# Optimization experiments

Hardware: AMD Instinct MI355X
Metric: run time of the kernel (lower is better)

The kernel has to match this reference:

```python
import jax, jax.numpy as jnp
import numpy as np

# config constants
H = 2048          # hidden_size
I_MOE = 1408      # moe_intermediate_size
E = 8             # n_routed_experts
TOP_K = 2         # num_experts_per_tok
NG = 4            # n_group
TOPK_G = 2        # topk_group
SCALE = 2.5       # routed_scaling_factor
N_SHARED = 2      # n_shared_experts
I_SHARED = I_MOE * N_SHARED
B, S = 1, 2048


def setup_inputs() -> dict:
    key = jax.random.key(0)
    ks = jax.random.split(key, 9)
    sc = 0.02
    return {
        "x": jax.random.normal(ks[0], (B, S, H), dtype=jnp.float32),
        "router_weight": jax.random.normal(ks[1], (E, H), dtype=jnp.float32) * sc,
        "e_score_correction_bias": jnp.zeros((E,), dtype=jnp.float32),
        "gate_w": jax.random.normal(ks[2], (E, I_MOE, H), dtype=jnp.float32) * sc,
        "up_w": jax.random.normal(ks[3], (E, I_MOE, H), dtype=jnp.float32) * sc,
        "down_w": jax.random.normal(ks[4], (E, H, I_MOE), dtype=jnp.float32) * sc,
        "shared_gate_w": jax.random.normal(ks[5], (I_SHARED, H), dtype=jnp.float32) * sc,
        "shared_up_w": jax.random.normal(ks[6], (I_SHARED, H), dtype=jnp.float32) * sc,
        "shared_down_w": jax.random.normal(ks[7], (H, I_SHARED), dtype=jnp.float32) * sc,
    }


def _mlp(x, gw, uw, dw):
    # SwiGLU MLP: down( silu(gate(x)) * up(x) )
    return (jax.nn.silu(x @ gw.T) * (x @ uw.T)) @ dw.T


def _route(x2d, rw, bias):
    T = x2d.shape[0]
    logits = x2d.astype(jnp.float32) @ rw.astype(jnp.float32).T          # [T,E]
    scores = jax.nn.sigmoid(logits)                                       # [T,E]
    sfc = scores + bias[None, :]                                          # [T,E]
    # group scores: sum of top-2 per group
    grp = sfc.reshape(T, NG, E // NG)
    group_scores = jnp.sum(jax.lax.top_k(grp, 2)[0], axis=-1)             # [T,NG]
    grp_idx = jax.lax.top_k(group_scores, TOPK_G)[1]                      # [T,topk_group]
    group_mask = jnp.zeros((T, NG), jnp.float32).at[
        jnp.arange(T)[:, None], grp_idx].set(1.0)                         # [T,NG]
    score_mask = jnp.repeat(group_mask, E // NG, axis=1)                  # [T,E]
    masked = jnp.where(score_mask > 0, sfc, 0.0)
    topk_idx = jax.lax.top_k(masked, TOP_K)[1]                            # [T,K]
    topk_w = jnp.take_along_axis(scores, topk_idx, axis=1)                # [T,K]
    topk_w = topk_w / (jnp.sum(topk_w, axis=-1, keepdims=True) + 1e-20)   # norm_topk_prob
    return topk_idx, topk_w * SCALE


def reference(x, router_weight, e_score_correction_bias, gate_w, up_w, down_w,
              shared_gate_w, shared_up_w, shared_down_w):
    orig_shape = x.shape
    x2d = x.reshape(-1, H)                                                # [T,H]
    T = x2d.shape[0]
    topk_idx, topk_w = _route(x2d, router_weight, e_score_correction_bias)
    # per-token per-expert combine weights [T,E] (top-k indices are distinct per token)
    cw = jnp.zeros((T, E), jnp.float32).at[
        jnp.arange(T)[:, None], topk_idx].add(topk_w)

    def expert_body(acc, ws):
        gw, uw, dw, cwe = ws  # gw/uw:[I,H], dw:[H,I], cwe:[T]
        y = _mlp(x2d, gw, uw, dw)
        return acc + cwe[:, None] * y, None

    routed, _ = jax.lax.scan(expert_body, jnp.zeros_like(x2d),
                             (gate_w, up_w, down_w, cw.T))
    out = routed.reshape(orig_shape) + _mlp(x, shared_gate_w, shared_up_w, shared_down_w)
    return out
```

## Files before the change

### kernel.cpp

```cpp
#include <hip/hip_runtime.h>
#include <hip/hip_bf16.h>
#include <math.h>

#define H 2048
#define IMOE 1408
#define NEXP 8
#define T_TOK 2048
#define ISH 2816
#define SCALEF 2.5f

#define NT_GU_R (IMOE / 64)
#define NT_GU_S (ISH / 64)
#define NT_DN   (H / 128)
#define GU_GRID (39 * NT_GU_R + 16 * NT_GU_S)
#define DN_GRID (39 * NT_DN + 16 * NT_DN)

typedef __attribute__((ext_vector_type(8))) short short8;
typedef __attribute__((ext_vector_type(4))) short short4v;
typedef __attribute__((ext_vector_type(4))) float floatx4;

__device__ inline float b2f(short v) {
    unsigned int u = ((unsigned int)(unsigned short)v) << 16;
    float f; __builtin_memcpy(&f, &u, 4); return f;
}
__device__ inline short f2b(float f) {
    __hip_bfloat16 h = __float2bfloat16(f);
    short s; __builtin_memcpy(&s, &h, 2); return s;
}

__device__ __forceinline__ void async16(const short* g, short* l) {
    __builtin_amdgcn_global_load_lds(
        (const __attribute__((address_space(1))) unsigned*)g,
        (__attribute__((address_space(3))) unsigned*)l, 16, 0, 0);
}

__device__ __forceinline__ int xcd_map(int orig, int nwg) {
    int q = nwg >> 3, r = nwg & 7;
    int x = orig & 7, s = orig >> 3;
    int base = (x < r) ? x * (q + 1) : r * (q + 1) + (x - r) * q;
    return base + s;
}

__global__ __launch_bounds__(256) void router_kernel(
    const float* __restrict__ x, const float* __restrict__ rw,
    const float* __restrict__ bias,
    int* __restrict__ cnt, int* __restrict__ tokList, int* __restrict__ slotList,
    float* __restrict__ pairW)
{
    const int wid  = (blockIdx.x * 256 + threadIdx.x) >> 6;
    const int lane = threadIdx.x & 63;
    if (wid >= T_TOK) return;
    const float* xr = x + (size_t)wid * H;

    float acc[NEXP];
#pragma unroll
    for (int e = 0; e < NEXP; ++e) acc[e] = 0.f;

#pragma unroll
    for (int c = 0; c < 8; ++c) {
        int idx = (c * 64 + lane) * 4;
        floatx4 xv = *(const floatx4*)(xr + idx);
#pragma unroll
        for (int e = 0; e < NEXP; ++e) {
            floatx4 wv = *(const floatx4*)(rw + e * H + idx);
            acc[e] += xv.x * wv.x + xv.y * wv.y + xv.z * wv.z + xv.w * wv.w;
        }
    }
#pragma unroll
    for (int e = 0; e < NEXP; ++e)
        for (int off = 32; off; off >>= 1)
            acc[e] += __shfl_xor(acc[e], off, 64);

    if (lane == 0) {
        float s[NEXP], sfc[NEXP];
#pragma unroll
        for (int e = 0; e < NEXP; ++e) {
            s[e]   = 1.0f / (1.0f + expf(-acc[e]));
            sfc[e] = s[e] + bias[e];
        }
        float gs[4];
#pragma unroll
        for (int g = 0; g < 4; ++g) gs[g] = sfc[2 * g] + sfc[2 * g + 1];
        int g1 = 0;
        for (int g = 1; g < 4; ++g) if (gs[g] > gs[g1]) g1 = g;
        int g2 = -1;
        for (int g = 0; g < 4; ++g) {
            if (g == g1) continue;
            if (g2 < 0 || gs[g] > gs[g2]) g2 = g;
        }
        float msk[NEXP];
#pragma unroll
        for (int e = 0; e < NEXP; ++e) {
            int g = e >> 1;
            msk[e] = (g == g1 || g == g2) ? sfc[e] : 0.0f;
        }
        int e1 = 0;
        for (int e = 1; e < NEXP; ++e) if (msk[e] > msk[e1]) e1 = e;
        int e2 = -1;
        for (int e = 0; e < NEXP; ++e) {
            if (e == e1) continue;
            if (e2 < 0 || msk[e] > msk[e2]) e2 = e;
        }
        float w1 = s[e1], w2 = s[e2];
        float inv = SCALEF / (w1 + w2 + 1e-20f);
        w1 *= inv; w2 *= inv;
        int p1 = atomicAdd(&cnt[e1], 1);
        tokList[e1 * T_TOK + p1]  = wid;
        slotList[e1 * T_TOK + p1] = 2 * wid;
        pairW[2 * wid] = w1;
        int p2 = atomicAdd(&cnt[e2], 1);
        tokList[e2 * T_TOK + p2]  = wid;
        slotList[e2 * T_TOK + p2] = 2 * wid + 1;
        pairW[2 * wid + 1] = w2;
    }
}

__global__ void plan_kernel(const int* __restrict__ cnt, int* __restrict__ meta)
{
    if (blockIdx.x != 0 || threadIdx.x != 0) return;
    int base = 0, gu = 0, dn = 0;
    meta[20] = 0; meta[32] = 0;
    for (int e = 0; e < NEXP; ++e) {
        int M = cnt[e];
        meta[e] = M;
        meta[9 + e] = base;
        base += M;
        int MT = (M + 127) >> 7;
        gu += MT * NT_GU_R;
        dn += MT * NT_DN;
        meta[21 + e] = gu;
        meta[33 + e] = dn;
    }
    meta[8]  = T_TOK;
    meta[17] = 0;
    meta[29] = gu + 16 * NT_GU_S;
    meta[41] = dn + 16 * NT_DN;
}

__global__ __launch_bounds__(256) void convert_kernel(
    const float* __restrict__ src, short* __restrict__ dst, int n4)
{
    int idx = blockIdx.x * 256 + threadIdx.x;
    int stride = gridDim.x * 256;
    for (; idx < n4; idx += stride) {
        floatx4 v = *(const floatx4*)(src + (size_t)idx * 4);
        short4v o = { f2b(v.x), f2b(v.y), f2b(v.z), f2b(v.w) };
        *(short4v*)(dst + (size_t)idx * 4) = o;
    }
}

#define W8_GU  2883584
#define W8_SH  720896
#define W8_S1  (W8_GU)
#define W8_S2  (2*W8_GU)
#define W8_S3  (3*W8_GU)
#define W8_S4  (3*W8_GU + W8_SH)
#define W8_S5  (3*W8_GU + 2*W8_SH)
#define W8_S6  (3*W8_GU + 3*W8_SH)
__global__ __launch_bounds__(256) void wconvert_kernel(
    const float* __restrict__ gw, const float* __restrict__ uw,
    const float* __restrict__ dw, const float* __restrict__ sgw,
    const float* __restrict__ suw, const float* __restrict__ sdw,
    short* __restrict__ gwb, short* __restrict__ uwb, short* __restrict__ dwb,
    short* __restrict__ sgwb, short* __restrict__ suwb, short* __restrict__ sdwb)
{
    int idx = blockIdx.x * 256 + threadIdx.x;
    int stride = gridDim.x * 256;
    for (; idx < W8_S6; idx += stride) {
        const float* s; short* d; int local;
        if (idx < W8_S3) {
            if (idx < W8_S1)      { s = gw;  d = gwb;  local = idx; }
            else if (idx < W8_S2) { s = uw;  d = uwb;  local = idx - W8_S1; }
            else                  { s = dw;  d = dwb;  local = idx - W8_S2; }
        } else {
            if (idx < W8_S4)      { s = sgw; d = sgwb; local = idx - W8_S3; }
            else if (idx < W8_S5) { s = suw; d = suwb; local = idx - W8_S4; }
            else                  { s = sdw; d = sdwb; local = idx - W8_S5; }
        }
        floatx4 v0 = *(const floatx4*)(s + (size_t)local * 8);
        floatx4 v1 = *(const floatx4*)(s + (size_t)local * 8 + 4);
        short8 o = { f2b(v0.x), f2b(v0.y), f2b(v0.z), f2b(v0.w),
                     f2b(v1.x), f2b(v1.y), f2b(v1.z), f2b(v1.w) };
        *(short8*)(d + (size_t)local * 8) = o;
    }
}

__global__ __launch_bounds__(256) void gu_gemm(
    const short* __restrict__ xb,
    const short* __restrict__ gwb, const short* __restrict__ uwb,
    const short* __restrict__ sgwb, const short* __restrict__ suwb,
    short* __restrict__ hiddenP, short* __restrict__ hiddenS,
    const int* __restrict__ tokList, const int* __restrict__ meta)
{
    const int total = meta[29];
    if (blockIdx.x >= total) return;
    const int idx = xcd_map(blockIdx.x, total);
    int e = 0;
    while (e < 8 && idx >= meta[21 + e]) ++e;

    int M, NT, Nout, rowBase;
    const short *b1, *b2;
    const int* gat;
    short* outP;
    if (e < 8) {
        M = meta[e]; NT = NT_GU_R; Nout = IMOE; rowBase = meta[9 + e];
        b1 = gwb + (size_t)e * IMOE * H;
        b2 = uwb + (size_t)e * IMOE * H;
        gat = tokList + e * T_TOK;
        outP = hiddenP;
    } else {
        M = T_TOK; NT = NT_GU_S; Nout = ISH; rowBase = 0;
        b1 = sgwb; b2 = suwb; gat = nullptr; outP = hiddenS;
    }
    const int MT = (M + 127) >> 7;
    const int local = idx - meta[20 + e];
    const int mt = local % MT;
    const int nt = local / MT;

    __shared__ short As[128 * 64];
    __shared__ short Bgu[128 * 64];

    const int tid  = threadIdx.x;
    const int w    = tid >> 6;
    const int lane = tid & 63;
    const int quad = lane >> 4;
    const int l16  = lane & 15;
    const int wm = w >> 1, wn = w & 1;

    const int r8 = lane >> 3;
    const int cs = (lane & 7) ^ r8;
    const short* aSrc[4];
    const short* bSrc[4];
    short* ldsA[4];
    short* ldsB[4];
#pragma unroll
    for (int i = 0; i < 4; ++i) {
        int r = w * 32 + i * 8 + r8;
        int p = mt * 128 + r;
        int pos = p < M ? p : (M - 1);
        int arow = gat ? gat[pos] : pos;
        aSrc[i] = xb + (size_t)arow * H + cs * 8;
        ldsA[i] = As + (w * 32 + i * 8) * 64;
        const short* wsrc = (r < 64) ? (b1 + (size_t)(nt * 64 + r) * H)
                                     : (b2 + (size_t)(nt * 64 + r - 64) * H);
        bSrc[i] = wsrc + cs * 8;
        ldsB[i] = Bgu + (w * 32 + i * 8) * 64;
    }

    floatx4 accg[4][2] = {};
    floatx4 accu[4][2] = {};

    for (int k0 = 0; k0 < H; k0 += 64) {
#pragma unroll
        for (int i = 0; i < 4; ++i) async16(aSrc[i] + k0, ldsA[i]);
#pragma unroll
        for (int i = 0; i < 4; ++i) async16(bSrc[i] + k0, ldsB[i]);
        __syncthreads();
        const int sw = l16 & 7;
        short8 af[4], bgf[2], buf[2];
#pragma unroll
        for (int kk2 = 0; kk2 < 2; ++kk2) {
            const int c = kk2 * 4 + quad;
#pragma unroll
            for (int m = 0; m < 4; ++m)
                af[m] = *(const short8*)(As + (wm * 64 + m * 16 + l16) * 64 + (c ^ sw) * 8);
#pragma unroll
            for (int n = 0; n < 2; ++n) {
                bgf[n] = *(const short8*)(Bgu + (wn * 32 + n * 16 + l16) * 64 + (c ^ sw) * 8);
                buf[n] = *(const short8*)(Bgu + (64 + wn * 32 + n * 16 + l16) * 64 + (c ^ sw) * 8);
            }
#pragma unroll
            for (int m = 0; m < 4; ++m)
#pragma unroll
                for (int n = 0; n < 2; ++n) {
                    accg[m][n] = __builtin_amdgcn_mfma_f32_16x16x32_bf16(af[m], bgf[n], accg[m][n], 0, 0, 0);
                    accu[m][n] = __builtin_amdgcn_mfma_f32_16x16x32_bf16(af[m], buf[n], accu[m][n], 0, 0, 0);
                }
        }
        __syncthreads();
    }

#pragma unroll
    for (int m = 0; m < 4; ++m) {
#pragma unroll
        for (int rr = 0; rr < 4; ++rr) {
            int lr = wm * 64 + m * 16 + quad * 4 + rr;
            int p = mt * 128 + lr;
            if (p >= M) continue;
            size_t rowoff = (size_t)(rowBase + p) * Nout + nt * 64 + wn * 32;
#pragma unroll
            for (int n = 0; n < 2; ++n) {
                float g = accg[m][n][rr];
                float u = accu[m][n][rr];
                outP[rowoff + n * 16 + l16] = f2b(g / (1.0f + __expf(-g)) * u);
            }
        }
    }
}

__global__ __launch_bounds__(256) void dn_gemm(
    const short* __restrict__ hiddenP, const short* __restrict__ hiddenS,
    const short* __restrict__ dwb, const short* __restrict__ sdwb,
    short* __restrict__ outPairs, short* __restrict__ sharedOut,
    const int* __restrict__ slotList, const int* __restrict__ meta)
{
    const int total = meta[41];
    if (blockIdx.x >= total) return;
    const int rtot = meta[40];
    int idx;
    if (blockIdx.x < rtot) idx = xcd_map(blockIdx.x, rtot);
    else                   idx = rtot + xcd_map(blockIdx.x - rtot, total - rtot);
    int e = 0;
    while (e < 8 && idx >= meta[33 + e]) ++e;

    int M, K, rowBase;
    const short* bp;
    const short* Abase;
    const int* scat;
    short* outP;
    if (e < 8) {
        M = meta[e]; K = IMOE; rowBase = meta[9 + e];
        bp = dwb + (size_t)e * H * IMOE;
        Abase = hiddenP; scat = slotList + e * T_TOK; outP = outPairs;
    } else {
        M = T_TOK; K = ISH; rowBase = 0;
        bp = sdwb; Abase = hiddenS; scat = nullptr; outP = sharedOut;
    }
    const int MT = (M + 127) >> 7;
    const int local = idx - meta[32 + e];
    const int mt = local % MT;
    const int nt = local / MT;

    __shared__ short As[128 * 64];
    __shared__ short Bs[128 * 64];

    const int tid  = threadIdx.x;
    const int w    = tid >> 6;
    const int lane = tid & 63;
    const int quad = lane >> 4;
    const int l16  = lane & 15;
    const int wm = w >> 1, wn = w & 1;

    const int r8 = lane >> 3;
    const int cs = (lane & 7) ^ r8;
    const short* aSrc[4];
    const short* bSrc[4];
    short* ldsA[4];
    short* ldsB[4];
#pragma unroll
    for (int i = 0; i < 4; ++i) {
        int r = w * 32 + i * 8 + r8;
        int p = mt * 128 + r;
        int pos = p < M ? p : (M - 1);
        aSrc[i] = Abase + (size_t)(rowBase + pos) * K + cs * 8;
        ldsA[i] = As + (w * 32 + i * 8) * 64;
        bSrc[i] = bp + (size_t)(nt * 128 + r) * K + cs * 8;
        ldsB[i] = Bs + (w * 32 + i * 8) * 64;
    }

    floatx4 acc[4][4] = {};

    const int kIters = K >> 6;
    for (int kt = 0; kt < kIters; ++kt) {
        const int k0 = kt << 6;
#pragma unroll
        for (int i = 0; i < 4; ++i) async16(aSrc[i] + k0, ldsA[i]);
#pragma unroll
        for (int i = 0; i < 4; ++i) async16(bSrc[i] + k0, ldsB[i]);
        __syncthreads();
        const int sw = l16 & 7;
        short8 af[4], bf[4];
#pragma unroll
        for (int kk2 = 0; kk2 < 2; ++kk2) {
            const int c = kk2 * 4 + quad;
#pragma unroll
            for (int m = 0; m < 4; ++m)
                af[m] = *(const short8*)(As + (wm * 64 + m * 16 + l16) * 64 + (c ^ sw) * 8);
#pragma unroll
            for (int n = 0; n < 4; ++n)
                bf[n] = *(const short8*)(Bs + (wn * 64 + n * 16 + l16) * 64 + (c ^ sw) * 8);
#pragma unroll
            for (int m = 0; m < 4; ++m)
#pragma unroll
                for (int n = 0; n < 4; ++n)
                    acc[m][n] = __builtin_amdgcn_mfma_f32_16x16x32_bf16(af[m], bf[n], acc[m][n], 0, 0, 0);
        }
        __syncthreads();
    }

#pragma unroll
    for (int m = 0; m < 4; ++m) {
#pragma unroll
        for (int rr = 0; rr < 4; ++rr) {
            int lr = wm * 64 + m * 16 + quad * 4 + rr;
            int p = mt * 128 + lr;
            if (p >= M) continue;
            int crow = scat ? scat[p] : p;
            size_t rowoff = (size_t)crow * H + nt * 128 + wn * 64;
#pragma unroll
            for (int n = 0; n < 4; ++n)
                outP[rowoff + n * 16 + l16] = f2b(acc[m][n][rr]);
        }
    }
}

__global__ __launch_bounds__(256) void combine_kernel(
    const short* __restrict__ outPairs, const short* __restrict__ sharedOut,
    const float* __restrict__ pairW, float* __restrict__ out)
{
    size_t gi = ((size_t)blockIdx.x * 256 + threadIdx.x) * 8;
    int t = (int)(gi >> 11);
    int h = (int)(gi & (H - 1));
    float w0 = pairW[2 * t], w1 = pairW[2 * t + 1];
    short8 p0 = *(const short8*)(outPairs + (size_t)(2 * t) * H + h);
    short8 p1 = *(const short8*)(outPairs + (size_t)(2 * t + 1) * H + h);
    short8 sh = *(const short8*)(sharedOut + gi);
    floatx4 o0, o1;
#pragma unroll
    for (int j = 0; j < 4; ++j)
        o0[j] = w0 * b2f(p0[j]) + w1 * b2f(p1[j]) + b2f(sh[j]);
#pragma unroll
    for (int j = 0; j < 4; ++j)
        o1[j] = w0 * b2f(p0[4 + j]) + w1 * b2f(p1[4 + j]) + b2f(sh[4 + j]);
    *(floatx4*)(out + gi)     = o0;
    *(floatx4*)(out + gi + 4) = o1;
}

extern "C" void kernel_launch(void* const* d_in, const int* in_sizes, int n_in,
                              void* d_out, int out_size, void* d_ws, size_t ws_size,
                              hipStream_t stream)
{
    const float* x    = (const float*)d_in[0];
    const float* rw   = (const float*)d_in[1];
    const float* bias = (const float*)d_in[2];
    const float* gw   = (const float*)d_in[3];
    const float* uw   = (const float*)d_in[4];
    const float* dw   = (const float*)d_in[5];
    const float* sgw  = (const float*)d_in[6];
    const float* suw  = (const float*)d_in[7];
    const float* sdw  = (const float*)d_in[8];
    float* out = (float*)d_out;

    char* ws = (char*)d_ws;
    size_t off = 0;
    auto alloc = [&](size_t bytes) {
        off = (off + 255) & ~(size_t)255;
        void* p = ws + off;
        off += bytes;
        return p;
    };
    int*   cnt       = (int*)  alloc(NEXP * sizeof(int));
    int*   tokList   = (int*)  alloc((size_t)NEXP * T_TOK * sizeof(int));
    int*   slotList  = (int*)  alloc((size_t)NEXP * T_TOK * sizeof(int));
    float* pairW     = (float*)alloc((size_t)2 * T_TOK * sizeof(float));
    int*   meta      = (int*)  alloc(64 * sizeof(int));
    short* xb        = (short*)alloc((size_t)T_TOK * H * sizeof(short));
    short* hiddenP   = (short*)alloc((size_t)2 * T_TOK * IMOE * sizeof(short));
    short* hiddenS   = (short*)alloc((size_t)T_TOK * ISH * sizeof(short));
    short* outPairs  = (short*)alloc((size_t)2 * T_TOK * H * sizeof(short));
    short* sharedOut = (short*)alloc((size_t)T_TOK * H * sizeof(short));
    short* gwb  = (short*)alloc((size_t)NEXP * IMOE * H * sizeof(short));
    short* uwb  = (short*)alloc((size_t)NEXP * IMOE * H * sizeof(short));
    short* dwb  = (short*)alloc((size_t)NEXP * H * IMOE * sizeof(short));
    short* sgwb = (short*)alloc((size_t)ISH * H * sizeof(short));
    short* suwb = (short*)alloc((size_t)ISH * H * sizeof(short));
    short* sdwb = (short*)alloc((size_t)H * ISH * sizeof(short));
    (void)ws_size;

    hipMemsetAsync(cnt, 0, NEXP * sizeof(int), stream);

    router_kernel<<<T_TOK / 4, 256, 0, stream>>>(x, rw, bias, cnt, tokList, slotList, pairW);
    plan_kernel<<<1, 64, 0, stream>>>(cnt, meta);
    convert_kernel<<<2048, 256, 0, stream>>>(x, xb, T_TOK * H / 4);
    wconvert_kernel<<<2048, 256, 0, stream>>>(gw, uw, dw, sgw, suw, sdw,
                                              gwb, uwb, dwb, sgwb, suwb, sdwb);

    gu_gemm<<<GU_GRID, 256, 0, stream>>>(xb, gwb, uwb, sgwb, suwb,
                                         hiddenP, hiddenS, tokList, meta);
    dn_gemm<<<DN_GRID, 256, 0, stream>>>(hiddenP, hiddenS, dwb, sdwb,
                                         outPairs, sharedOut, slotList, meta);

    combine_kernel<<<(T_TOK * H / 8) / 256, 256, 0, stream>>>(outPairs, sharedOut, pairW, out);
}
```

Baseline: 657.6 us.

## Double-buffer LDS tiles in gate/up and down GEMMs with async prefetch

Both GEMM kernels now keep two LDS buffers and issue the async global-to-LDS loads for the next K tile before computing on the current one. Explicit vmcnt waits and raw barriers replace the __syncthreads pairs, so each wait covers only the older tile's loads. The aim is to hide global load latency behind MFMA work. In exchange, LDS use per block doubles, which may cut occupancy, and correctness depends on the hand-counted vmcnt value matching the 8 loads issued per iteration.

```diff
diff --git a/kernel.cpp b/kernel.cpp
--- a/kernel.cpp
+++ b/kernel.cpp
@@ -14,6 +14,7 @@
 #define NT_DN   (H / 128)
 #define GU_GRID (39 * NT_GU_R + 16 * NT_GU_S)
 #define DN_GRID (39 * NT_DN + 16 * NT_DN)
+#define LDS_HALF (128 * 64)
 
 typedef __attribute__((ext_vector_type(8))) short short8;
 typedef __attribute__((ext_vector_type(4))) short short4v;
@@ -217,8 +218,8 @@
     const int mt = local % MT;
     const int nt = local / MT;
 
-    __shared__ short As[128 * 64];
-    __shared__ short Bgu[128 * 64];
+    __shared__ short As[2 * LDS_HALF];
+    __shared__ short Bgu[2 * LDS_HALF];
 
     const int tid  = threadIdx.x;
     const int w    = tid >> 6;
@@ -250,12 +251,27 @@
     floatx4 accg[4][2] = {};
     floatx4 accu[4][2] = {};
 
+#pragma unroll
+    for (int i = 0; i < 4; ++i) { async16(aSrc[i], ldsA[i]); async16(bSrc[i], ldsB[i]); }
+
+    int cur = 0;
     for (int k0 = 0; k0 < H; k0 += 64) {
-#pragma unroll
-        for (int i = 0; i < 4; ++i) async16(aSrc[i] + k0, ldsA[i]);
-#pragma unroll
-        for (int i = 0; i < 4; ++i) async16(bSrc[i] + k0, ldsB[i]);
-        __syncthreads();
+        const int nk = k0 + 64;
+        if (nk < H) {
+            const int noff = (cur ^ 1) * LDS_HALF;
+#pragma unroll
+            for (int i = 0; i < 4; ++i) {
+                async16(aSrc[i] + nk, ldsA[i] + noff);
+                async16(bSrc[i] + nk, ldsB[i] + noff);
+            }
+            asm volatile("s_waitcnt vmcnt(8)" ::: "memory");
+        } else {
+            asm volatile("s_waitcnt vmcnt(0)" ::: "memory");
+        }
+        __builtin_amdgcn_s_barrier();
+
+        const short* Ab = As  + cur * LDS_HALF;
+        const short* Bb = Bgu + cur * LDS_HALF;
         const int sw = l16 & 7;
         short8 af[4], bgf[2], buf[2];
 #pragma unroll
@@ -263,11 +279,11 @@
             const int c = kk2 * 4 + quad;
 #pragma unroll
             for (int m = 0; m < 4; ++m)
-                af[m] = *(const short8*)(As + (wm * 64 + m * 16 + l16) * 64 + (c ^ sw) * 8);
+                af[m] = *(const short8*)(Ab + (wm * 64 + m * 16 + l16) * 64 + (c ^ sw) * 8);
 #pragma unroll
             for (int n = 0; n < 2; ++n) {
-                bgf[n] = *(const short8*)(Bgu + (wn * 32 + n * 16 + l16) * 64 + (c ^ sw) * 8);
-                buf[n] = *(const short8*)(Bgu + (64 + wn * 32 + n * 16 + l16) * 64 + (c ^ sw) * 8);
+                bgf[n] = *(const short8*)(Bb + (wn * 32 + n * 16 + l16) * 64 + (c ^ sw) * 8);
+                buf[n] = *(const short8*)(Bb + (64 + wn * 32 + n * 16 + l16) * 64 + (c ^ sw) * 8);
             }
 #pragma unroll
             for (int m = 0; m < 4; ++m)
@@ -277,7 +293,8 @@
                     accu[m][n] = __builtin_amdgcn_mfma_f32_16x16x32_bf16(af[m], buf[n], accu[m][n], 0, 0, 0);
                 }
         }
-        __syncthreads();
+        __builtin_amdgcn_s_barrier();
+        cur ^= 1;
     }
 
 #pragma unroll
@@ -331,8 +348,8 @@
     const int mt = local % MT;
     const int nt = local / MT;
 
-    __shared__ short As[128 * 64];
-    __shared__ short Bs[128 * 64];
+    __shared__ short As[2 * LDS_HALF];
+    __shared__ short Bs[2 * LDS_HALF];
 
     const int tid  = threadIdx.x;
     const int w    = tid >> 6;
@@ -360,14 +377,28 @@
 
     floatx4 acc[4][4] = {};
 
+#pragma unroll
+    for (int i = 0; i < 4; ++i) { async16(aSrc[i], ldsA[i]); async16(bSrc[i], ldsB[i]); }
+
     const int kIters = K >> 6;
+    int cur = 0;
     for (int kt = 0; kt < kIters; ++kt) {
-        const int k0 = kt << 6;
-#pragma unroll
-        for (int i = 0; i < 4; ++i) async16(aSrc[i] + k0, ldsA[i]);
-#pragma unroll
-        for (int i = 0; i < 4; ++i) async16(bSrc[i] + k0, ldsB[i]);
-        __syncthreads();
+        const int nk = (kt + 1) << 6;
+        if (kt + 1 < kIters) {
+            const int noff = (cur ^ 1) * LDS_HALF;
+#pragma unroll
+            for (int i = 0; i < 4; ++i) {
+                async16(aSrc[i] + nk, ldsA[i] + noff);
+                async16(bSrc[i] + nk, ldsB[i] + noff);
+            }
+            asm volatile("s_waitcnt vmcnt(8)" ::: "memory");
+        } else {
+            asm volatile("s_waitcnt vmcnt(0)" ::: "memory");
+        }
+        __builtin_amdgcn_s_barrier();
+
+        const short* Ab = As + cur * LDS_HALF;
+        const short* Bb = Bs + cur * LDS_HALF;
         const int sw = l16 & 7;
         short8 af[4], bf[4];
 #pragma unroll
@@ -375,17 +406,18 @@
             const int c = kk2 * 4 + quad;
 #pragma unroll
             for (int m = 0; m < 4; ++m)
-                af[m] = *(const short8*)(As + (wm * 64 + m * 16 + l16) * 64 + (c ^ sw) * 8);
+                af[m] = *(const short8*)(Ab + (wm * 64 + m * 16 + l16) * 64 + (c ^ sw) * 8);
 #pragma unroll
             for (int n = 0; n < 4; ++n)
-                bf[n] = *(const short8*)(Bs + (wn * 64 + n * 16 + l16) * 64 + (c ^ sw) * 8);
+                bf[n] = *(const short8*)(Bb + (wn * 64 + n * 16 + l16) * 64 + (c ^ sw) * 8);
 #pragma unroll
             for (int m = 0; m < 4; ++m)
 #pragma unroll
                 for (int n = 0; n < 4; ++n)
                     acc[m][n] = __builtin_amdgcn_mfma_f32_16x16x32_bf16(af[m], bf[n], acc[m][n], 0, 0, 0);
         }
-        __syncthreads();
+        __builtin_amdgcn_s_barrier();
+        cur ^= 1;
     }
 
 #pragma unroll
```

Measured after the change: 653.0 us. About the same (-0.7%).

## Fuse router with x/weight conversion and overlap down-weight conversion with gate-up GEMM

Applied to the files above, without the earlier changes.

The router kernel now also writes the bf16 copy of x and, through extra blocks, converts the gate/up and shared gate/up weights. The down-projection weight conversion moves into spare blocks appended to the gate-up GEMM grid, so it runs alongside that GEMM. Per-expert token lists are now built by a deterministic prefix-scan kernel instead of global atomics, which also removes the memset. This cuts kernel launches and serialized conversion passes, at the cost of extra blocks competing with the GEMM for bandwidth and compute.

```diff
diff --git a/kernel.cpp b/kernel.cpp
--- a/kernel.cpp
+++ b/kernel.cpp
@@ -15,6 +15,11 @@
 #define GU_GRID (39 * NT_GU_R + 16 * NT_GU_S)
 #define DN_GRID (39 * NT_DN + 16 * NT_DN)
 
+#define W8_GU  2883584
+#define W8_SH  720896
+#define GUW8   (2 * W8_GU + 2 * W8_SH)
+#define DNW8   (W8_GU + W8_SH)
+
 typedef __attribute__((ext_vector_type(8))) short short8;
 typedef __attribute__((ext_vector_type(4))) short short4v;
 typedef __attribute__((ext_vector_type(4))) float floatx4;
@@ -41,16 +46,40 @@
     return base + s;
 }
 
-__global__ __launch_bounds__(256) void router_kernel(
+__device__ __forceinline__ void cvt8(const float* s, short* d, size_t local) {
+    floatx4 v0 = *(const floatx4*)(s + local * 8);
+    floatx4 v1 = *(const floatx4*)(s + local * 8 + 4);
+    short8 o = { f2b(v0.x), f2b(v0.y), f2b(v0.z), f2b(v0.w),
+                 f2b(v1.x), f2b(v1.y), f2b(v1.z), f2b(v1.w) };
+    *(short8*)(d + local * 8) = o;
+}
+
+__global__ __launch_bounds__(256) void route_conv_kernel(
     const float* __restrict__ x, const float* __restrict__ rw,
     const float* __restrict__ bias,
-    int* __restrict__ cnt, int* __restrict__ tokList, int* __restrict__ slotList,
-    float* __restrict__ pairW)
-{
+    float* __restrict__ pairW, int2* __restrict__ pickE, short* __restrict__ xb,
+    const float* __restrict__ gw, const float* __restrict__ uw,
+    const float* __restrict__ sgw, const float* __restrict__ suw,
+    short* __restrict__ gwb, short* __restrict__ uwb,
+    short* __restrict__ sgwb, short* __restrict__ suwb)
+{
+    if (blockIdx.x >= 512) {
+        int u = (blockIdx.x - 512) * 256 + threadIdx.x;
+        for (; u < GUW8; u += 2048 * 256) {
+            const float* s; short* d; int local;
+            if (u < W8_GU)               { s = gw;  d = gwb;  local = u; }
+            else if (u < 2 * W8_GU)      { s = uw;  d = uwb;  local = u - W8_GU; }
+            else if (u < 2 * W8_GU + W8_SH) { s = sgw; d = sgwb; local = u - 2 * W8_GU; }
+            else                         { s = suw; d = suwb; local = u - 2 * W8_GU - W8_SH; }
+            cvt8(s, d, (size_t)local);
+        }
+        return;
+    }
+
     const int wid  = (blockIdx.x * 256 + threadIdx.x) >> 6;
     const int lane = threadIdx.x & 63;
-    if (wid >= T_TOK) return;
     const float* xr = x + (size_t)wid * H;
+    short* xbrow = xb + (size_t)wid * H;
 
     float acc[NEXP];
 #pragma unroll
@@ -65,6 +94,8 @@
             floatx4 wv = *(const floatx4*)(rw + e * H + idx);
             acc[e] += xv.x * wv.x + xv.y * wv.y + xv.z * wv.z + xv.w * wv.w;
         }
+        short4v o = { f2b(xv.x), f2b(xv.y), f2b(xv.z), f2b(xv.w) };
+        *(short4v*)(xbrow + idx) = o;
     }
 #pragma unroll
     for (int e = 0; e < NEXP; ++e)
@@ -103,16 +134,45 @@
         }
         float w1 = s[e1], w2 = s[e2];
         float inv = SCALEF / (w1 + w2 + 1e-20f);
-        w1 *= inv; w2 *= inv;
-        int p1 = atomicAdd(&cnt[e1], 1);
-        tokList[e1 * T_TOK + p1]  = wid;
-        slotList[e1 * T_TOK + p1] = 2 * wid;
-        pairW[2 * wid] = w1;
-        int p2 = atomicAdd(&cnt[e2], 1);
-        tokList[e2 * T_TOK + p2]  = wid;
-        slotList[e2 * T_TOK + p2] = 2 * wid + 1;
-        pairW[2 * wid + 1] = w2;
-    }
+        pairW[2 * wid]     = w1 * inv;
+        pairW[2 * wid + 1] = w2 * inv;
+        int2 pk; pk.x = e1; pk.y = e2;
+        pickE[wid] = pk;
+    }
+}
+
+__global__ __launch_bounds__(256) void build_lists(
+    const int2* __restrict__ pickE, int* __restrict__ cnt,
+    int* __restrict__ tokList, int* __restrict__ slotList)
+{
+    const int e = blockIdx.x;
+    const int tid = threadIdx.x;
+    __shared__ int pre[256];
+    const int t0 = tid * 8;
+    int2 p[8];
+#pragma unroll
+    for (int j = 0; j < 8; ++j) p[j] = pickE[t0 + j];
+    int cme = 0;
+#pragma unroll
+    for (int j = 0; j < 8; ++j) cme += (p[j].x == e || p[j].y == e) ? 1 : 0;
+    pre[tid] = cme;
+    __syncthreads();
+    for (int off = 1; off < 256; off <<= 1) {
+        int v = (tid >= off) ? pre[tid - off] : 0;
+        __syncthreads();
+        pre[tid] += v;
+        __syncthreads();
+    }
+    int base = pre[tid] - cme;
+#pragma unroll
+    for (int j = 0; j < 8; ++j) {
+        if (p[j].x == e || p[j].y == e) {
+            tokList[e * T_TOK + base]  = t0 + j;
+            slotList[e * T_TOK + base] = 2 * (t0 + j) + (p[j].x == e ? 0 : 1);
+            ++base;
+        }
+    }
+    if (tid == 255) cnt[e] = pre[255];
 }
 
 __global__ void plan_kernel(const int* __restrict__ cnt, int* __restrict__ meta)
@@ -137,63 +197,26 @@
     meta[41] = dn + 16 * NT_DN;
 }
 
-__global__ __launch_bounds__(256) void convert_kernel(
-    const float* __restrict__ src, short* __restrict__ dst, int n4)
-{
-    int idx = blockIdx.x * 256 + threadIdx.x;
-    int stride = gridDim.x * 256;
-    for (; idx < n4; idx += stride) {
-        floatx4 v = *(const floatx4*)(src + (size_t)idx * 4);
-        short4v o = { f2b(v.x), f2b(v.y), f2b(v.z), f2b(v.w) };
-        *(short4v*)(dst + (size_t)idx * 4) = o;
-    }
-}
-
-#define W8_GU  2883584
-#define W8_SH  720896
-#define W8_S1  (W8_GU)
-#define W8_S2  (2*W8_GU)
-#define W8_S3  (3*W8_GU)
-#define W8_S4  (3*W8_GU + W8_SH)
-#define W8_S5  (3*W8_GU + 2*W8_SH)
-#define W8_S6  (3*W8_GU + 3*W8_SH)
-__global__ __launch_bounds__(256) void wconvert_kernel(
-    const float* __restrict__ gw, const float* __restrict__ uw,
-    const float* __restrict__ dw, const float* __restrict__ sgw,
-    const float* __restrict__ suw, const float* __restrict__ sdw,
-    short* __restrict__ gwb, short* __restrict__ uwb, short* __restrict__ dwb,
-    short* __restrict__ sgwb, short* __restrict__ suwb, short* __restrict__ sdwb)
-{
-    int idx = blockIdx.x * 256 + threadIdx.x;
-    int stride = gridDim.x * 256;
-    for (; idx < W8_S6; idx += stride) {
-        const float* s; short* d; int local;
-        if (idx < W8_S3) {
-            if (idx < W8_S1)      { s = gw;  d = gwb;  local = idx; }
-            else if (idx < W8_S2) { s = uw;  d = uwb;  local = idx - W8_S1; }
-            else                  { s = dw;  d = dwb;  local = idx - W8_S2; }
-        } else {
-            if (idx < W8_S4)      { s = sgw; d = sgwb; local = idx - W8_S3; }
-            else if (idx < W8_S5) { s = suw; d = suwb; local = idx - W8_S4; }
-            else                  { s = sdw; d = sdwb; local = idx - W8_S5; }
-        }
-        floatx4 v0 = *(const floatx4*)(s + (size_t)local * 8);
-        floatx4 v1 = *(const floatx4*)(s + (size_t)local * 8 + 4);
-        short8 o = { f2b(v0.x), f2b(v0.y), f2b(v0.z), f2b(v0.w),
-                     f2b(v1.x), f2b(v1.y), f2b(v1.z), f2b(v1.w) };
-        *(short8*)(d + (size_t)local * 8) = o;
-    }
-}
-
 __global__ __launch_bounds__(256) void gu_gemm(
     const short* __restrict__ xb,
     const short* __restrict__ gwb, const short* __restrict__ uwb,
     const short* __restrict__ sgwb, const short* __restrict__ suwb,
     short* __restrict__ hiddenP, short* __restrict__ hiddenS,
-    const int* __restrict__ tokList, const int* __restrict__ meta)
+    const int* __restrict__ tokList, const int* __restrict__ meta,
+    const float* __restrict__ dw, const float* __restrict__ sdw,
+    short* __restrict__ dwb, short* __restrict__ sdwb)
 {
     const int total = meta[29];
-    if (blockIdx.x >= total) return;
+    if (blockIdx.x >= total) {
+        int rid = blockIdx.x - total;
+        if (rid >= 512) return;
+        int u = rid * 256 + threadIdx.x;
+        for (; u < DNW8; u += 512 * 256) {
+            if (u < W8_GU) cvt8(dw, dwb, (size_t)u);
+            else           cvt8(sdw, sdwb, (size_t)(u - W8_GU));
+        }
+        return;
+    }
     const int idx = xcd_map(blockIdx.x, total);
     int e = 0;
     while (e < 8 && idx >= meta[21 + e]) ++e;
@@ -453,6 +476,7 @@
     int*   tokList   = (int*)  alloc((size_t)NEXP * T_TOK * sizeof(int));
     int*   slotList  = (int*)  alloc((size_t)NEXP * T_TOK * sizeof(int));
     float* pairW     = (float*)alloc((size_t)2 * T_TOK * sizeof(float));
+    int2*  pickE     = (int2*) alloc((size_t)T_TOK * sizeof(int2));
     int*   meta      = (int*)  alloc(64 * sizeof(int));
     short* xb        = (short*)alloc((size_t)T_TOK * H * sizeof(short));
     short* hiddenP   = (short*)alloc((size_t)2 * T_TOK * IMOE * sizeof(short));
@@ -467,16 +491,15 @@
     short* sdwb = (short*)alloc((size_t)H * ISH * sizeof(short));
     (void)ws_size;
 
-    hipMemsetAsync(cnt, 0, NEXP * sizeof(int), stream);
-
-    router_kernel<<<T_TOK / 4, 256, 0, stream>>>(x, rw, bias, cnt, tokList, slotList, pairW);
+    route_conv_kernel<<<2560, 256, 0, stream>>>(x, rw, bias, pairW, pickE, xb,
+                                                gw, uw, sgw, suw,
+                                                gwb, uwb, sgwb, suwb);
+    build_lists<<<NEXP, 256, 0, stream>>>(pickE, cnt, tokList, slotList);
     plan_kernel<<<1, 64, 0, stream>>>(cnt, meta);
-    convert_kernel<<<2048, 256, 0, stream>>>(x, xb, T_TOK * H / 4);
-    wconvert_kernel<<<2048, 256, 0, stream>>>(gw, uw, dw, sgw, suw, sdw,
-                                              gwb, uwb, dwb, sgwb, suwb, sdwb);
-
-    gu_gemm<<<GU_GRID, 256, 0, stream>>>(xb, gwb, uwb, sgwb, suwb,
-                                         hiddenP, hiddenS, tokList, meta);
+
+    gu_gemm<<<GU_GRID + 512, 256, 0, stream>>>(xb, gwb, uwb, sgwb, suwb,
+                                               hiddenP, hiddenS, tokList, meta,
+                                               dw, sdw, dwb, sdwb);
     dn_gemm<<<DN_GRID, 256, 0, stream>>>(hiddenP, hiddenS, dwb, sdwb,
                                          outPairs, sharedOut, slotList, meta);
 
```

Result: faster. 579.4 us (-11.9%).
